# Kernel tuning notes

Measured on AMD Instinct MI355X. Metric: run time of the kernel, lower is better.

## Reference

```python
import jax, jax.numpy as jnp
import numpy as np

B, C, H, W, N = 32, 256, 56, 56, 1024


def setup_inputs() -> dict:
    key = jax.random.key(0)
    k1, k2, k3, k4 = jax.random.split(key, 4)
    x = jax.random.normal(k1, (B, C, H, W), dtype=jnp.float32)
    W_s = jax.random.normal(k2, (N, H, W), dtype=jnp.float32)
    W_d = jax.random.normal(k3, (N, C, 1, 1), dtype=jnp.float32)
    W_b = jax.random.normal(k4, (1, N), dtype=jnp.float32)
    return {"x": x, "W_s": W_s, "W_d": W_d, "W_b": W_b}


def reference(x, W_s, W_d, W_b):
    # Original: out = einsum('bchw,nhw->bnchw'); per-neuron 1x1 conv with W_d[n]
    # (C -> 1 channel); sum over (c,h,w); add bias. Mathematically:
    #   out[b,n] = sum_{c,h,w} x[b,c,h,w] * W_s[n,h,w] * W_d[n,c] + W_b[0,n]
    # Computed without materializing the (B,N,C,H,W) blow-up:
    y = jnp.einsum('bchw,nhw->bnc', x, W_s)          # spatial contraction
    out = jnp.einsum('bnc,nc->bn', y, W_d[:, :, 0, 0])  # channel contraction
    return out + W_b
```

## Files before the change

### kernel.cpp

```cpp
#include <hip/hip_runtime.h>
#include <stdint.h>


#define K_DIM 3136
#define N_DIM 1024
#define C_DIM 256
#define B_DIM 32
#define M_DIM 8192
#define X_ELEMS (M_DIM * K_DIM)
#define WS_ELEMS (N_DIM * K_DIM)
#define NSTEP 49

typedef __attribute__((ext_vector_type(8))) short short8v;
typedef __attribute__((ext_vector_type(4))) float f32x4;

__device__ __forceinline__ short f2bf(float f) {
  union { float f; unsigned u; } v; v.f = f;
  unsigned r = v.u + 0x7FFFu + ((v.u >> 16) & 1u);
  return (short)(r >> 16);
}

__device__ __forceinline__ void async16(const void* g, void* l) {
  __builtin_amdgcn_global_load_lds(
      (const __attribute__((address_space(1))) unsigned int*)g,
      (__attribute__((address_space(3))) unsigned int*)l, 16, 0, 0);
}

#define XBLK (X_ELEMS / 4096)
#define CVBLK ((X_ELEMS + WS_ELEMS) / 4096)
__global__ __launch_bounds__(256) void convert_bf16_bias(
    const float* __restrict__ x, const float* __restrict__ Ws,
    const float* __restrict__ Wb, short* __restrict__ dst,
    float* __restrict__ out) {
  int bid = blockIdx.x;
  if (bid >= CVBLK) {
    int i = (bid - CVBLK) * 256 + threadIdx.x;
    out[i] = Wb[i & (N_DIM - 1)];
    return;
  }
  const float* src;
  short* d;
  size_t base;
  if (bid < XBLK) {
    src = x; d = dst; base = (size_t)bid * 4096;
  } else {
    src = Ws; d = dst + X_ELEMS; base = (size_t)(bid - XBLK) * 4096;
  }
#pragma unroll
  for (int h = 0; h < 2; ++h) {
    size_t i = base + threadIdx.x * 8 + h * 2048;
    f32x4 v0 = __builtin_nontemporal_load((const f32x4*)(src + i));
    f32x4 v1 = __builtin_nontemporal_load((const f32x4*)(src + i) + 1);
    short8v s;
    s[0] = f2bf(v0.x); s[1] = f2bf(v0.y); s[2] = f2bf(v0.z); s[3] = f2bf(v0.w);
    s[4] = f2bf(v1.x); s[5] = f2bf(v1.y); s[6] = f2bf(v1.z); s[7] = f2bf(v1.w);
    *(short8v*)(d + i) = s;
  }
}


#define VMCNT(N) asm volatile("s_waitcnt vmcnt(" #N ")" ::: "memory")
#define CBAR() asm volatile("" ::: "memory")
#define BARR() { CBAR(); __builtin_amdgcn_s_barrier(); CBAR(); }

#define STAGEA(T) { char* d_ = sm + (((T) & 3) << 15) + (wv << 10);           \
    const short* g_ = Ag + (size_t)(T) * 32;                                  \
    async16(g_, d_);                                                          \
    async16(g_ + (size_t)128 * K_DIM, d_ + 8192); }

#define STAGEB(T) { char* d_ = sm + (((T) & 3) << 15) + 16384 + (wv << 10);   \
    const short* g_ = Bg + (size_t)(T) * 32;                                  \
    async16(g_, d_);                                                          \
    async16(g_ + (size_t)128 * K_DIM, d_ + 8192); }

#define MFQ(F, AV)                                                            \
  acc[F][0] = __builtin_amdgcn_mfma_f32_16x16x32_bf16(AV, b0, acc[F][0], 0, 0, 0); \
  acc[F][1] = __builtin_amdgcn_mfma_f32_16x16x32_bf16(AV, b1, acc[F][1], 0, 0, 0); \
  acc[F][2] = __builtin_amdgcn_mfma_f32_16x16x32_bf16(AV, b2, acc[F][2], 0, 0, 0); \
  acc[F][3] = __builtin_amdgcn_mfma_f32_16x16x32_bf16(AV, b3, acc[F][3], 0, 0, 0);

#define KTILE(T, STG, VMSTMT)                                                 \
  {                                                                           \
    char* sl = sm + (((T) & 3) << 15);                                        \
    if (STG) STAGEA((T) + 3);                                                 \
    short8v b0 = *(const short8v*)(sl + boff);                                \
    short8v b1 = *(const short8v*)(sl + boff + 1024);                         \
    short8v b2 = *(const short8v*)(sl + boff + 2048);                         \
    short8v b3 = *(const short8v*)(sl + boff + 3072);                         \
    short8v a0 = *(const short8v*)(sl + aoff);                                \
    short8v a1 = *(const short8v*)(sl + aoff + 1024);                         \
    short8v a2 = *(const short8v*)(sl + aoff + 2048);                         \
    short8v a3 = *(const short8v*)(sl + aoff + 3072);                         \
    BARR();                                                                   \
    __builtin_amdgcn_s_setprio(1);                                            \
    MFQ(0, a0) MFQ(1, a1) MFQ(2, a2) MFQ(3, a3)                               \
    __builtin_amdgcn_s_setprio(0);                                            \
    BARR();                                                                   \
    if (STG) STAGEB((T) + 3);                                                 \
    a0 = *(const short8v*)(sl + aoff + 4096);                                 \
    a1 = *(const short8v*)(sl + aoff + 5120);                                 \
    a2 = *(const short8v*)(sl + aoff + 6144);                                 \
    a3 = *(const short8v*)(sl + aoff + 7168);                                 \
    VMSTMT;                                                                   \
    __builtin_amdgcn_sched_barrier(0);                                        \
    BARR();                                                                   \
    __builtin_amdgcn_s_setprio(1);                                            \
    MFQ(4, a0) MFQ(5, a1) MFQ(6, a2) MFQ(7, a3)                               \
    __builtin_amdgcn_s_setprio(0);                                            \
    BARR();                                                                   \
  }

__global__ __launch_bounds__(512, 2) void gemm_fused(
    const short* __restrict__ Abf, const short* __restrict__ Bbf,
    const float* __restrict__ Wd, float* __restrict__ out) {
  __shared__ __align__(16) char sm[131072];

  const int bid = blockIdx.x;
  const int mt = bid & 31;
  const int nt = (bid >> 5) & 3;
  const int z = bid >> 7;
  const int kt0 = z * NSTEP;

  const int tid = threadIdx.x;
  const int lane = tid & 63;
  const int wv = tid >> 6;
  const int r = lane & 15;
  const int q = lane >> 4;
  const int wm = wv >> 2, wn = wv & 3;

  const int srow = wv * 16 + (lane >> 2);
  const int sk8 = (lane & 3) ^ ((lane >> 3) & 3);
  const short* Ag = Abf + (size_t)(mt * 256 + srow) * K_DIM + kt0 * 32 + sk8 * 8;
  const short* Bg = Bbf + (size_t)(nt * 256 + srow) * K_DIM + kt0 * 32 + sk8 * 8;

  const int swz = (q ^ ((r >> 1) & 3)) << 4;
  const int aoff = (wm * 128 + r) * 64 + swz;
  const int boff = 16384 + (wn * 64 + r) * 64 + swz;

  f32x4 acc[8][4];
#pragma unroll
  for (int i = 0; i < 8; ++i)
#pragma unroll
    for (int j = 0; j < 4; ++j) acc[i][j] = (f32x4)0.0f;

  STAGEA(0) STAGEB(0) STAGEA(1) STAGEB(1) STAGEA(2) STAGEB(2)
  VMCNT(8);
  BARR();

#pragma unroll 1
  for (int t = 0; t < NSTEP - 3; ++t) KTILE(t, 1, VMCNT(8));
  KTILE(NSTEP - 3, 0, VMCNT(4));
  KTILE(NSTEP - 2, 0, VMCNT(0));
  KTILE(NSTEP - 1, 0, (void)0);

#pragma unroll
  for (int j = 0; j < 4; ++j) {
    const int n_g = nt * 256 + wn * 64 + 16 * j + r;
    float p = 0.0f;
#pragma unroll
    for (int i = 0; i < 8; ++i) {
      const int c_l = wm * 128 + 16 * i + 4 * q;
      const float4 wd = *(const float4*)(Wd + (size_t)n_g * C_DIM + c_l);
      p += acc[i][j].x * wd.x + acc[i][j].y * wd.y + acc[i][j].z * wd.z +
           acc[i][j].w * wd.w;
    }
    p += __shfl_xor(p, 16, 64);
    p += __shfl_xor(p, 32, 64);
    if (q == 0) atomicAdd(&out[(size_t)mt * N_DIM + n_g], p);
  }
}

extern "C" void kernel_launch(void* const* d_in, const int* in_sizes, int n_in,
                              void* d_out, int out_size, void* d_ws, size_t ws_size,
                              hipStream_t stream) {
  const float* x = (const float*)d_in[0];
  const float* Ws = (const float*)d_in[1];
  const float* Wd = (const float*)d_in[2];
  const float* Wb = (const float*)d_in[3];
  float* out = (float*)d_out;
  short* xbf = (short*)d_ws;

  convert_bf16_bias<<<dim3(CVBLK + 128), dim3(256), 0, stream>>>(x, Ws, Wb, xbf, out);
  gemm_fused<<<dim3(32 * 4 * 2), dim3(512), 0, stream>>>(xbf, xbf + X_ELEMS, Wd, out);
}
```

Baseline: 209.6 us.

## Shrink GEMM tile to 256x128 with 3-slot LDS ring for higher occupancy

Measured after the change: 228.2 us. 8.9% more time.

```diff
diff --git a/kernel.cpp b/kernel.cpp
--- a/kernel.cpp
+++ b/kernel.cpp
@@ -5,11 +5,12 @@
 #define K_DIM 3136
 #define N_DIM 1024
 #define C_DIM 256
-#define B_DIM 32
 #define M_DIM 8192
 #define X_ELEMS (M_DIM * K_DIM)
 #define WS_ELEMS (N_DIM * K_DIM)
 #define NSTEP 49
+#define SLOT 24576
+#define LDS_BYTES (3 * SLOT)
 
 typedef __attribute__((ext_vector_type(8))) short short8v;
 typedef __attribute__((ext_vector_type(4))) float f32x4;
@@ -60,65 +61,53 @@
 
 
 #define VMCNT(N) asm volatile("s_waitcnt vmcnt(" #N ")" ::: "memory")
+#define LGKM0() asm volatile("s_waitcnt lgkmcnt(0)" ::: "memory")
+#define SB0() __builtin_amdgcn_sched_barrier(0)
 #define CBAR() asm volatile("" ::: "memory")
 #define BARR() { CBAR(); __builtin_amdgcn_s_barrier(); CBAR(); }
 
-#define STAGEA(T) { char* d_ = sm + (((T) & 3) << 15) + (wv << 10);           \
-    const short* g_ = Ag + (size_t)(T) * 32;                                  \
-    async16(g_, d_);                                                          \
-    async16(g_ + (size_t)128 * K_DIM, d_ + 8192); }
+#define STAGE(T, SO) {                                                        \
+    char* d_ = sm + (SO) + (wv << 10);                                        \
+    const short* ga_ = Ag + (size_t)(T) * 32;                                 \
+    async16(ga_, d_);                                                         \
+    async16(ga_ + (size_t)128 * K_DIM, d_ + 8192);                            \
+    async16(Bg + (size_t)(T) * 32, d_ + 16384); }
 
-#define STAGEB(T) { char* d_ = sm + (((T) & 3) << 15) + 16384 + (wv << 10);   \
-    const short* g_ = Bg + (size_t)(T) * 32;                                  \
-    async16(g_, d_);                                                          \
-    async16(g_ + (size_t)128 * K_DIM, d_ + 8192); }
+#define M16(A, B, C) __builtin_amdgcn_mfma_f32_16x16x32_bf16(A, B, C, 0, 0, 0)
 
-#define MFQ(F, AV)                                                            \
-  acc[F][0] = __builtin_amdgcn_mfma_f32_16x16x32_bf16(AV, b0, acc[F][0], 0, 0, 0); \
-  acc[F][1] = __builtin_amdgcn_mfma_f32_16x16x32_bf16(AV, b1, acc[F][1], 0, 0, 0); \
-  acc[F][2] = __builtin_amdgcn_mfma_f32_16x16x32_bf16(AV, b2, acc[F][2], 0, 0, 0); \
-  acc[F][3] = __builtin_amdgcn_mfma_f32_16x16x32_bf16(AV, b3, acc[F][3], 0, 0, 0);
-
-#define KTILE(T, STG, VMSTMT)                                                 \
+#define KBODY(CO)                                                             \
   {                                                                           \
-    char* sl = sm + (((T) & 3) << 15);                                        \
-    if (STG) STAGEA((T) + 3);                                                 \
+    const char* sl = sm + (CO);                                               \
+    short8v a0 = *(const short8v*)(sl + aoff);                                \
+    short8v a1 = *(const short8v*)(sl + aoff + 1024);                         \
+    short8v a2 = *(const short8v*)(sl + aoff + 2048);                         \
+    short8v a3 = *(const short8v*)(sl + aoff + 3072);                         \
     short8v b0 = *(const short8v*)(sl + boff);                                \
     short8v b1 = *(const short8v*)(sl + boff + 1024);                         \
     short8v b2 = *(const short8v*)(sl + boff + 2048);                         \
     short8v b3 = *(const short8v*)(sl + boff + 3072);                         \
-    short8v a0 = *(const short8v*)(sl + aoff);                                \
-    short8v a1 = *(const short8v*)(sl + aoff + 1024);                         \
-    short8v a2 = *(const short8v*)(sl + aoff + 2048);                         \
-    short8v a3 = *(const short8v*)(sl + aoff + 3072);                         \
-    BARR();                                                                   \
+    SB0();                                                                    \
     __builtin_amdgcn_s_setprio(1);                                            \
-    MFQ(0, a0) MFQ(1, a1) MFQ(2, a2) MFQ(3, a3)                               \
+    acc[0][0]=M16(a0,b0,acc[0][0]); acc[1][0]=M16(a1,b0,acc[1][0]);           \
+    acc[2][0]=M16(a2,b0,acc[2][0]); acc[3][0]=M16(a3,b0,acc[3][0]);           \
+    acc[0][1]=M16(a0,b1,acc[0][1]); acc[1][1]=M16(a1,b1,acc[1][1]);           \
+    acc[2][1]=M16(a2,b1,acc[2][1]); acc[3][1]=M16(a3,b1,acc[3][1]);           \
+    acc[0][2]=M16(a0,b2,acc[0][2]); acc[1][2]=M16(a1,b2,acc[1][2]);           \
+    acc[2][2]=M16(a2,b2,acc[2][2]); acc[3][2]=M16(a3,b2,acc[3][2]);           \
+    acc[0][3]=M16(a0,b3,acc[0][3]); acc[1][3]=M16(a1,b3,acc[1][3]);           \
+    acc[2][3]=M16(a2,b3,acc[2][3]); acc[3][3]=M16(a3,b3,acc[3][3]);           \
     __builtin_amdgcn_s_setprio(0);                                            \
-    BARR();                                                                   \
-    if (STG) STAGEB((T) + 3);                                                 \
-    a0 = *(const short8v*)(sl + aoff + 4096);                                 \
-    a1 = *(const short8v*)(sl + aoff + 5120);                                 \
-    a2 = *(const short8v*)(sl + aoff + 6144);                                 \
-    a3 = *(const short8v*)(sl + aoff + 7168);                                 \
-    VMSTMT;                                                                   \
-    __builtin_amdgcn_sched_barrier(0);                                        \
-    BARR();                                                                   \
-    __builtin_amdgcn_s_setprio(1);                                            \
-    MFQ(4, a0) MFQ(5, a1) MFQ(6, a2) MFQ(7, a3)                               \
-    __builtin_amdgcn_s_setprio(0);                                            \
-    BARR();                                                                   \
   }
 
-__global__ __launch_bounds__(512, 2) void gemm_fused(
+__global__ __launch_bounds__(512, 4) void gemm_fused(
     const short* __restrict__ Abf, const short* __restrict__ Bbf,
     const float* __restrict__ Wd, float* __restrict__ out) {
-  __shared__ __align__(16) char sm[131072];
+  __shared__ __align__(16) char sm[LDS_BYTES];
 
   const int bid = blockIdx.x;
-  const int mt = bid & 31;
-  const int nt = (bid >> 5) & 3;
-  const int z = bid >> 7;
+  const int nt = bid & 7;
+  const int mt = (bid >> 3) & 31;
+  const int z = bid >> 8;
   const int kt0 = z * NSTEP;
 
   const int tid = threadIdx.x;
@@ -126,40 +115,51 @@
   const int wv = tid >> 6;
   const int r = lane & 15;
   const int q = lane >> 4;
-  const int wm = wv >> 2, wn = wv & 3;
+  const int wm = wv >> 1, wn = wv & 1;
 
   const int srow = wv * 16 + (lane >> 2);
   const int sk8 = (lane & 3) ^ ((lane >> 3) & 3);
   const short* Ag = Abf + (size_t)(mt * 256 + srow) * K_DIM + kt0 * 32 + sk8 * 8;
-  const short* Bg = Bbf + (size_t)(nt * 256 + srow) * K_DIM + kt0 * 32 + sk8 * 8;
+  const short* Bg = Bbf + (size_t)(nt * 128 + srow) * K_DIM + kt0 * 32 + sk8 * 8;
 
   const int swz = (q ^ ((r >> 1) & 3)) << 4;
-  const int aoff = (wm * 128 + r) * 64 + swz;
+  const int aoff = (wm * 64 + r) * 64 + swz;
   const int boff = 16384 + (wn * 64 + r) * 64 + swz;
 
-  f32x4 acc[8][4];
+  f32x4 acc[4][4];
 #pragma unroll
-  for (int i = 0; i < 8; ++i)
+  for (int i = 0; i < 4; ++i)
 #pragma unroll
     for (int j = 0; j < 4; ++j) acc[i][j] = (f32x4)0.0f;
 
-  STAGEA(0) STAGEB(0) STAGEA(1) STAGEB(1) STAGEA(2) STAGEB(2)
-  VMCNT(8);
+  STAGE(0, 0) STAGE(1, SLOT)
+  VMCNT(3);
   BARR();
 
+  unsigned co = 0, so = 2 * SLOT;
 #pragma unroll 1
-  for (int t = 0; t < NSTEP - 3; ++t) KTILE(t, 1, VMCNT(8));
-  KTILE(NSTEP - 3, 0, VMCNT(4));
-  KTILE(NSTEP - 2, 0, VMCNT(0));
-  KTILE(NSTEP - 1, 0, (void)0);
+  for (int t = 0; t < NSTEP - 2; ++t) {
+    STAGE(t + 2, so)
+    KBODY(co)
+    VMCNT(3);
+    LGKM0();
+    BARR();
+    co += SLOT; if (co == LDS_BYTES) co = 0;
+    so += SLOT; if (so == LDS_BYTES) so = 0;
+  }
+  KBODY(co)
+  VMCNT(0);
+  BARR();
+  co += SLOT; if (co == LDS_BYTES) co = 0;
+  KBODY(co)
 
 #pragma unroll
   for (int j = 0; j < 4; ++j) {
-    const int n_g = nt * 256 + wn * 64 + 16 * j + r;
+    const int n_g = nt * 128 + wn * 64 + 16 * j + r;
     float p = 0.0f;
 #pragma unroll
-    for (int i = 0; i < 8; ++i) {
-      const int c_l = wm * 128 + 16 * i + 4 * q;
+    for (int i = 0; i < 4; ++i) {
+      const int c_l = wm * 64 + 16 * i + 4 * q;
       const float4 wd = *(const float4*)(Wd + (size_t)n_g * C_DIM + c_l);
       p += acc[i][j].x * wd.x + acc[i][j].y * wd.y + acc[i][j].z * wd.z +
            acc[i][j].w * wd.w;
@@ -181,5 +181,5 @@
   short* xbf = (short*)d_ws;
 
   convert_bf16_bias<<<dim3(CVBLK + 128), dim3(256), 0, stream>>>(x, Ws, Wb, xbf, out);
-  gemm_fused<<<dim3(32 * 4 * 2), dim3(512), 0, stream>>>(xbf, xbf + X_ELEMS, Wd, out);
+  gemm_fused<<<dim3(512), dim3(512), 0, stream>>>(xbf, xbf + X_ELEMS, Wd, out);
 }
```
